# Optimization experiments

Hardware: AMD Instinct MI355X
Metric: run time of the kernel (lower is better)

Reference implementation:

```python
import jax, jax.numpy as jnp
import numpy as np

B, L, D, K, H = 2, 384, 1024, 128, 32
NUM_EDGES = 25600
NUM_T = 1000
SCALING = K ** -0.5
SQRT_2PI = float(np.sqrt(2.0 * np.pi))


def setup_inputs() -> dict:
    key = jax.random.key(0)
    ks = jax.random.split(key, 20)
    s = 0.02
    inp = {}
    inp["token_id"] = jax.random.randint(ks[0], (B, L), 0, 160)
    inp["is_periodic"] = jnp.zeros((B,), dtype=bool)
    inp["pos"] = 5.0 * jax.random.normal(ks[1], (B, L, 3), dtype=jnp.float32)
    inp["adj"] = jnp.ones((B, L, L), dtype=bool)
    inp["node_type_edge"] = jax.random.randint(ks[2], (B, L, L, 2), 0, NUM_EDGES)
    inp["time_step"] = jax.random.uniform(ks[3], (B, L), dtype=jnp.float32)
    inp["clean_mask"] = jnp.zeros((B, L), dtype=bool)
    # parameters
    inp["embed_w"] = s * jax.random.normal(ks[4], (160, D), dtype=jnp.float32)
    inp["Wpos"] = s * jax.random.normal(ks[5], (K, 3), dtype=jnp.float32)
    inp["Wpfe"] = s * jax.random.normal(ks[6], (D, K), dtype=jnp.float32)
    inp["gbf_means"] = jax.random.normal(ks[7], (K,), dtype=jnp.float32)
    inp["gbf_stds"] = 0.5 + jax.random.uniform(ks[8], (K,), dtype=jnp.float32)
    inp["gbf_mul"] = 1.0 + s * jax.random.normal(ks[9], (NUM_EDGES, 1), dtype=jnp.float32)
    inp["gbf_bias"] = s * jax.random.normal(ks[10], (NUM_EDGES, 1), dtype=jnp.float32)
    inp["W1"] = s * jax.random.normal(ks[11], (K, K), dtype=jnp.float32)
    inp["b1"] = jnp.zeros((K,), dtype=jnp.float32)
    inp["W2"] = s * jax.random.normal(ks[12], (H, K), dtype=jnp.float32)
    inp["b2"] = jnp.zeros((H,), dtype=jnp.float32)
    inp["Wproj"] = s * jax.random.normal(ks[13], (D, K), dtype=jnp.float32)
    inp["bproj"] = jnp.zeros((D,), dtype=jnp.float32)
    inp["Wt1"] = s * jax.random.normal(ks[14], (D, D), dtype=jnp.float32)
    inp["bt1"] = jnp.zeros((D,), dtype=jnp.float32)
    inp["Wt2"] = s * jax.random.normal(ks[15], (D, D), dtype=jnp.float32)
    inp["bt2"] = jnp.zeros((D,), dtype=jnp.float32)
    return inp


def _forward(token_id, is_periodic, pos, adj, node_type_edge, time_step, clean_mask,
             embed_w, Wpos, Wpfe, gbf_means, gbf_stds, gbf_mul, gbf_bias,
             W1, b1, W2, b2, Wproj, bproj, Wt1, bt1, Wt2, bt2):
    padding_mask = token_id == 0                                  # (B,L)
    molecule_mask = (token_id <= 129) & (~is_periodic[:, None])   # (B,L)
    x = embed_w[token_id]                                         # (B,L,D)

    # ---- _pos_emb (non-PBC branch: expand_pos = pos, expand_mask = padding_mask) ----
    delta = pos[:, :, None, :] - pos[:, None, :, :]               # (B,L,L,3)
    dist = jnp.sqrt(jnp.maximum(jnp.sum(delta * delta, -1), 1e-12))  # (B,L,L), safe norm

    # GaussianLayer
    mul = gbf_mul[node_type_edge].sum(-2)                         # (B,L,L,1)
    bias = gbf_bias[node_type_edge].sum(-2)                       # (B,L,L,1)
    y = mul * dist[..., None] + bias                              # (B,L,L,1) -> broadcast K
    std = jnp.abs(gbf_stds) + 1e-5
    a = (y - gbf_means) / std
    edge_feature = jnp.exp(-0.5 * a * a) / (SQRT_2PI * std)       # (B,L,L,K)

    # NonLinear projection to per-head bias
    gab = jax.nn.gelu(edge_feature @ W1.T + b1, approximate=False) @ W2.T + b2  # (B,L,L,H)
    gab = jnp.where(padding_mask[:, None, :, None], -jnp.inf, gab)  # expand-col mask
    gab = jnp.where(padding_mask[:, :, None, None], 0.0, gab)       # padding-row mask
    pos_attn_bias = jnp.transpose(gab, (0, 3, 1, 2))              # (B,H,L,L)

    d = gab.sum(-1)                                               # (B,L,L) sum over heads
    minv = jnp.finfo(jnp.float32).min
    d = jnp.where(padding_mask[:, None, :], minv, d)
    d = jnp.where(padding_mask[:, :, None], minv, d)
    adj_eff = adj | (~molecule_mask[:, :, None])
    d = jnp.where(~adj_eff, minv, d)
    attn = jax.nn.softmax(d * SCALING, axis=-1)                   # (B,L,L)

    pos_e = pos @ Wpos.T                                          # (B,L,K)
    pos_e = jnp.where(padding_mask[..., None], 0.0, pos_e)
    pfe = jnp.einsum('bij,bjk->bik', attn, pos_e)                 # (B,L,K)
    pfe = pfe @ Wpfe.T                                            # (B,L,D)

    ef = jnp.where(padding_mask[:, None, :, None], 0.0, edge_feature).sum(-2)  # (B,L,K)
    pfe = pfe + ef @ Wproj.T + bproj
    pos_embedding = jnp.where(padding_mask[..., None], 0.0, pfe)  # (B,L,D)

    # ---- time step encoder (sinusoidal + MLP) ----
    t = jnp.where(clean_mask, 0.0, time_step) * NUM_T             # (B,L)
    half = D // 2
    freqs = jnp.exp(-jnp.log(10000.0) * jnp.arange(half, dtype=jnp.float32) / half)
    ang = t[..., None] * freqs                                    # (B,L,half)
    sin_emb = jnp.concatenate([jnp.sin(ang), jnp.cos(ang)], -1)   # (B,L,D)
    time_embed = jax.nn.silu(sin_emb @ Wt1.T + bt1) @ Wt2.T + bt2

    x = x + time_embed + pos_embedding
    return x, padding_mask, time_embed, pos_attn_bias, pos_embedding


def reference(token_id, is_periodic, pos, adj, node_type_edge, time_step, clean_mask,
              embed_w, Wpos, Wpfe, gbf_means, gbf_stds, gbf_mul, gbf_bias,
              W1, b1, W2, b2, Wproj, bproj, Wt1, bt1, Wt2, bt2):
    return _forward(token_id, is_periodic, pos, adj, node_type_edge, time_step, clean_mask,
                    embed_w, Wpos, Wpfe, gbf_means, gbf_stds, gbf_mul, gbf_bias,
                    W1, b1, W2, b2, Wproj, bproj, Wt1, bt1, Wt2, bt2)
```

## Files before the change

### kernel.cpp

```cpp
#include <hip/hip_runtime.h>
#include <stddef.h>

#define B_ 2
#define L_ 384
#define D_ 1024
#define K_ 128
#define H_ 32

#define MINV (-3.402823466e38f)
#define NEG_BIG (-1.0e38f)
#define SCALING_ 0.08838834764831845f
#define INV_SQRT_2PI 0.3989422804014327f

typedef __attribute__((ext_vector_type(8))) short bf16x8;
typedef __attribute__((ext_vector_type(4))) float f32x4;

__device__ __forceinline__ float finitize(float x) {
    return fminf(fmaxf(x, -1.0e38f), 1.0e38f);
}
__device__ __forceinline__ unsigned short f2bf(float x) {
    unsigned int u = __float_as_uint(x);
    u += 0x7FFFu + ((u >> 16) & 1u);
    return (unsigned short)(u >> 16);
}
__device__ __forceinline__ unsigned short f2bf_rtz(float x) {
    return (unsigned short)(__float_as_uint(x) >> 16);
}
__device__ __forceinline__ float gelu_tanh(float x) {
    const float x2 = x * x;
    const float z = x * fmaf(0.0356774081f, x2, 0.7978845608f);
    const float e = __expf(2.0f * z);
    const float t = fmaf(-2.0f, __builtin_amdgcn_rcpf(e + 1.0f), 1.0f);
    const float hx = 0.5f * x;
    return fmaf(hx, t, hx);
}

__global__ __launch_bounds__(256) void prep_sin_kernel(
    const float* __restrict__ W1, const float* __restrict__ W2,
    const float* __restrict__ Wpfe, const float* __restrict__ Wproj,
    const float* __restrict__ Wt2,
    unsigned short* __restrict__ W1bf, unsigned short* __restrict__ W2bf,
    unsigned short* __restrict__ Wpfebf, unsigned short* __restrict__ Wprojbf,
    unsigned short* __restrict__ Wt2bf,
    const float* __restrict__ time_step, const unsigned char* __restrict__ clean,
    const int* __restrict__ token, unsigned short* __restrict__ sin_bf,
    float* __restrict__ padout)
{
    const int blk = blockIdx.x;
    if (blk < 1300) {
        const int i = blk * 256 + threadIdx.x;
        const float* src; unsigned short* dst; int off;
        if (i < 4096)       { src = W1;    dst = W1bf;    off = i; }
        else if (i < 5120)  { src = W2;    dst = W2bf;    off = i - 4096; }
        else if (i < 37888) { src = Wpfe;  dst = Wpfebf;  off = i - 5120; }
        else if (i < 70656) { src = Wproj; dst = Wprojbf; off = i - 37888; }
        else                { src = Wt2;   dst = Wt2bf;   off = i - 70656; }
        const float4 v = ((const float4*)src)[off];
        ushort4 p; p.x = f2bf(v.x); p.y = f2bf(v.y); p.z = f2bf(v.z); p.w = f2bf(v.w);
        ((ushort4*)dst)[off] = p;
    } else {
        const int row = blk - 1300;
        if (threadIdx.x == 0) padout[row] = (token[row] == 0) ? 1.0f : 0.0f;
        const float t = (clean[row] ? 0.0f : time_step[row]) * 1000.0f;
        for (int k = threadIdx.x; k < 512; k += 256) {
            const float f = __expf(-9.210340371976184f * (float)k * (1.0f / 512.0f));
            const float ang = t * f;
            sin_bf[(size_t)row * D_ + k]       = f2bf(__sinf(ang));
            sin_bf[(size_t)row * D_ + 512 + k] = f2bf(__cosf(ang));
        }
    }
}

__device__ __forceinline__ void gemm_ts_body(
    char* smem, int m0, int n0,
    const unsigned short* __restrict__ A, const float* __restrict__ Bw,
    const float* __restrict__ bias, void* __restrict__ Cv,
    int N, int Kd, int act)
{
    unsigned short (*sA)[72] = (unsigned short(*)[72])smem;
    unsigned short (*sB)[72] = (unsigned short(*)[72])(smem + 4608);
    const int tid  = threadIdx.x;
    const int lane = tid & 63;
    const int wave = tid >> 6;
    const int l15  = lane & 15;
    const int quad = lane >> 4;
    const int mt   = wave & 1;
    const int np   = wave >> 1;

    const int ar = tid >> 3, ac = (tid & 7) * 8;
    const int bc4 = (tid & 15) * 4;

    f32x4 acc[2];
#pragma unroll
    for (int t = 0; t < 2; ++t) acc[t] = (f32x4){0.f, 0.f, 0.f, 0.f};

    uint4 ra = *(const uint4*)&A[(size_t)(m0 + ar) * Kd + ac];
    float4 rbv[4];
#pragma unroll
    for (int c = 0; c < 4; ++c)
        rbv[c] = *(const float4*)&Bw[(size_t)(n0 + ((tid + c * 256) >> 4)) * Kd + bc4];

    for (int k0 = 0; k0 < Kd; k0 += 64) {
        *(uint4*)&sA[ar][ac] = ra;
#pragma unroll
        for (int c = 0; c < 4; ++c) {
            ushort4 p;
            p.x = f2bf(rbv[c].x); p.y = f2bf(rbv[c].y);
            p.z = f2bf(rbv[c].z); p.w = f2bf(rbv[c].w);
            *(ushort4*)&sB[(tid + c * 256) >> 4][bc4] = p;
        }
        __syncthreads();
        if (k0 + 64 < Kd) {
            ra = *(const uint4*)&A[(size_t)(m0 + ar) * Kd + k0 + 64 + ac];
#pragma unroll
            for (int c = 0; c < 4; ++c)
                rbv[c] = *(const float4*)&Bw[(size_t)(n0 + ((tid + c * 256) >> 4)) * Kd + k0 + 64 + bc4];
        }
#pragma unroll
        for (int kk = 0; kk < 64; kk += 32) {
            const bf16x8 av = *(const bf16x8*)&sA[mt * 16 + l15][kk + quad * 8];
#pragma unroll
            for (int t = 0; t < 2; ++t) {
                const bf16x8 bv = *(const bf16x8*)&sB[(np * 2 + t) * 16 + l15][kk + quad * 8];
                acc[t] = __builtin_amdgcn_mfma_f32_16x16x32_bf16(av, bv, acc[t], 0, 0, 0);
            }
        }
        __syncthreads();
    }
#pragma unroll
    for (int t = 0; t < 2; ++t) {
        const int nc = n0 + (np * 2 + t) * 16 + l15;
        const float bv = bias[nc];
#pragma unroll
        for (int r = 0; r < 4; ++r) {
            const int mr = m0 + mt * 16 + quad * 4 + r;
            float v = acc[t][r] + bv;
            if (act) {
                v = v / (1.0f + __expf(-v));
                ((unsigned short*)Cv)[(size_t)mr * N + nc] = f2bf(v);
            } else {
                ((float*)Cv)[(size_t)mr * N + nc] = v;
            }
        }
    }
}

__device__ __forceinline__ void edge_body(
    char* smem, int row,
    const int* __restrict__ token_id,
    const unsigned char* __restrict__ is_periodic,
    const float* __restrict__ pos,
    const unsigned char* __restrict__ adj,
    const int* __restrict__ nte,
    const float* __restrict__ gbf_means,
    const float* __restrict__ gbf_stds,
    const float* __restrict__ gbf_mul,
    const float* __restrict__ gbf_bias,
    const float* __restrict__ b1,
    const float* __restrict__ b2,
    const float* __restrict__ Wpos,
    const unsigned short* __restrict__ W1bf,
    const unsigned short* __restrict__ W2bf,
    unsigned short* __restrict__ pfe_bf,
    unsigned short* __restrict__ ef_bf,
    float* __restrict__ out_pab)
{
    const int b = row / L_;
    const int i = row - b * L_;
    const int tid = threadIdx.x;

    const int tok_i = token_id[row];
    if (tok_i == 0) {
        for (int idx = tid; idx < H_ * L_; idx += 256) {
            const int h = idx / L_;
            const int j = idx - h * L_;
            out_pab[((size_t)(b * H_ + h) * L_ + i) * L_ + j] = 0.0f;
        }
        if (tid < K_) {
            pfe_bf[(size_t)row * K_ + tid] = 0;
            ef_bf[(size_t)row * K_ + tid]  = 0;
        }
        return;
    }

    typedef unsigned short efbuf_t[32][136];
    efbuf_t* sEF = (efbuf_t*)smem;
    unsigned short (*sACT)[136] = (unsigned short(*)[136])(smem + 17408);
    float (*sGab)[33] = (float(*)[33])(smem + 26112);
    float* sD      = (float*)(smem + 30336);
    float* sRed    = (float*)(smem + 31872);
    float* sYall   = (float*)(smem + 32896);
    unsigned char* sPadCol = (unsigned char*)(smem + 34432);

    for (int j = tid; j < L_; j += 256)
        sPadCol[j] = (token_id[b * L_ + j] == 0) ? 1 : 0;

    const float px = pos[(size_t)row * 3 + 0];
    const float py = pos[(size_t)row * 3 + 1];
    const float pz = pos[(size_t)row * 3 + 2];
    for (int jg2 = tid; jg2 < L_; jg2 += 256) {
        const float dx = px - pos[(size_t)(b * L_ + jg2) * 3 + 0];
        const float dy = py - pos[(size_t)(b * L_ + jg2) * 3 + 1];
        const float dz = pz - pos[(size_t)(b * L_ + jg2) * 3 + 2];
        const float dist = sqrtf(fmaxf(dx * dx + dy * dy + dz * dz, 1e-12f));
        const size_t eoff = ((size_t)(b * L_ + i) * L_ + jg2) * 2;
        const int e0 = nte[eoff], e1 = nte[eoff + 1];
        sYall[jg2] = (gbf_mul[e0] + gbf_mul[e1]) * dist + (gbf_bias[e0] + gbf_bias[e1]);
    }

    const int lane = tid & 63;
    const int wave = tid >> 6;
    const int l15  = lane & 15;
    const int quad = lane >> 4;
    const int mt   = wave & 1;
    const int ntb  = (wave >> 1) * 4;
    float rb1[4];
#pragma unroll
    for (int nt = 0; nt < 4; ++nt) rb1[nt] = b1[(ntb + nt) * 16 + l15];
    const int hc = (wave >> 1) * 16 + l15;
    const float rb2 = b2[hc];
    bf16x8 w1f[4][4];
#pragma unroll
    for (int ks = 0; ks < 4; ++ks)
#pragma unroll
        for (int nt = 0; nt < 4; ++nt)
            w1f[ks][nt] = *(const bf16x8*)&W1bf[((ntb + nt) * 16 + l15) * K_ + ks * 32 + quad * 8];
    bf16x8 bv2[4];
#pragma unroll
    for (int ks = 0; ks < 4; ++ks)
        bv2[ks] = *(const bf16x8*)&W2bf[hc * K_ + ks * 32 + quad * 8];

    const int kg4 = (tid & 31) * 4;
    const int jg  = tid >> 5;
    const int jb  = jg * 4;
    float meanv[4], istdv[4], cKv[4];
#pragma unroll
    for (int c = 0; c < 4; ++c) {
        meanv[c] = gbf_means[kg4 + c];
        const float s = fabsf(gbf_stds[kg4 + c]) + 1e-5f;
        istdv[c] = 1.0f / s;
        cKv[c]   = INV_SQRT_2PI * istdv[c];
    }
    float efs[4] = {0.f, 0.f, 0.f, 0.f};

    __syncthreads();

#pragma unroll
    for (int jj = 0; jj < 4; ++jj) {
        const int j = jb + jj;
        const float y = sYall[j];
        const bool ok = !sPadCol[j];
        ushort4 p;
#pragma unroll
        for (int c = 0; c < 4; ++c) {
            const float a = (y - meanv[c]) * istdv[c];
            const float ef = __expf(-0.5f * a * a) * cKv[c];
            ((unsigned short*)&p)[c] = f2bf_rtz(ef);
            if (ok) efs[c] += ef;
        }
        *(ushort4*)&sEF[0][j][kg4] = p;
    }
    __syncthreads();

    for (int tile = 0; tile < L_ / 32; ++tile) {
        const int jt0 = tile * 32;
        const int cur = tile & 1, nxt = cur ^ 1;

        f32x4 acc1[4];
#pragma unroll
        for (int nt = 0; nt < 4; ++nt) acc1[nt] = (f32x4){0.f, 0.f, 0.f, 0.f};
#pragma unroll
        for (int ks = 0; ks < 4; ++ks) {
            const bf16x8 av = *(const bf16x8*)&sEF[cur][mt * 16 + l15][ks * 32 + quad * 8];
#pragma unroll
            for (int nt = 0; nt < 4; ++nt)
                acc1[nt] = __builtin_amdgcn_mfma_f32_16x16x32_bf16(av, w1f[ks][nt], acc1[nt], 0, 0, 0);
        }

        if (tile + 1 < L_ / 32) {
            const int jn0 = jt0 + 32;
#pragma unroll
            for (int jj = 0; jj < 4; ++jj) {
                const int j = jb + jj;
                const float y = sYall[jn0 + j];
                const bool ok = !sPadCol[jn0 + j];
                ushort4 p;
#pragma unroll
                for (int c = 0; c < 4; ++c) {
                    const float a = (y - meanv[c]) * istdv[c];
                    const float ef = __expf(-0.5f * a * a) * cKv[c];
                    ((unsigned short*)&p)[c] = f2bf_rtz(ef);
                    if (ok) efs[c] += ef;
                }
                *(ushort4*)&sEF[nxt][j][kg4] = p;
            }
        }

#pragma unroll
        for (int nt = 0; nt < 4; ++nt) {
            const int kkc = (ntb + nt) * 16 + l15;
#pragma unroll
            for (int r = 0; r < 4; ++r) {
                const float v = gelu_tanh(acc1[nt][r] + rb1[nt]);
                sACT[mt * 16 + quad * 4 + r][kkc] = f2bf_rtz(v);
            }
        }
        __syncthreads();

        f32x4 acc2 = (f32x4){0.f, 0.f, 0.f, 0.f};
#pragma unroll
        for (int ks = 0; ks < 4; ++ks) {
            const bf16x8 av = *(const bf16x8*)&sACT[mt * 16 + l15][ks * 32 + quad * 8];
            acc2 = __builtin_amdgcn_mfma_f32_16x16x32_bf16(av, bv2[ks], acc2, 0, 0, 0);
        }
        const int jl0 = mt * 16 + quad * 4;
#pragma unroll
        for (int r = 0; r < 4; ++r) sGab[jl0 + r][hc] = acc2[r] + rb2;
        __syncthreads();

        {
            const int h = tid >> 3, f = tid & 7;
            const int jb2 = f * 4;
            float4 st;
#pragma unroll
            for (int r = 0; r < 4; ++r) {
                float v = finitize(sGab[jb2 + r][h]);
                if (sPadCol[jt0 + jb2 + r]) v = NEG_BIG;
                ((float*)&st)[r] = v;
            }
            *(float4*)&out_pab[((size_t)(b * H_ + h) * L_ + i) * L_ + jt0 + jb2] = st;
        }
        if (tid < 32) {
            float s = 0.0f;
#pragma unroll
            for (int h = 0; h < 32; ++h) s += sGab[tid][h];
            sD[jt0 + tid] = s;
        }
    }

    {
        float* efScr = (float*)sACT;
#pragma unroll
        for (int c = 0; c < 4; ++c) efScr[jg * 128 + kg4 + c] = efs[c];
    }
    __syncthreads();
    if (tid < 128) {
        const float* efScr = (const float*)sACT;
        float s = 0.0f;
#pragma unroll
        for (int g = 0; g < 8; ++g) s += efScr[g * 128 + tid];
        ef_bf[(size_t)row * K_ + tid] = f2bf(s);
    }
    __syncthreads();

    const bool molecule = (tok_i <= 129) && (is_periodic[b] == 0);
    float lmax = -INFINITY;
    for (int j = tid; j < L_; j += 256) {
        const bool colpad = sPadCol[j] != 0;
        const bool adj_eff = (adj[((size_t)(b * L_ + i)) * L_ + j] != 0) || (!molecule);
        const float dv = (colpad || !adj_eff) ? MINV : sD[j];
        const float s = dv * SCALING_;
        sD[j] = s;
        lmax = fmaxf(lmax, s);
    }
#pragma unroll
    for (int off = 32; off > 0; off >>= 1) lmax = fmaxf(lmax, __shfl_xor(lmax, off));
    if (lane == 0) sRed[wave] = lmax;
    __syncthreads();
    const float smax = fmaxf(fmaxf(sRed[0], sRed[1]), fmaxf(sRed[2], sRed[3]));
    float lsum = 0.0f;
    for (int j = tid; j < L_; j += 256) {
        const float e = __expf(sD[j] - smax);
        sD[j] = e;
        lsum += e;
    }
#pragma unroll
    for (int off = 32; off > 0; off >>= 1) lsum += __shfl_xor(lsum, off);
    if (lane == 0) sRed[4 + wave] = lsum;
    __syncthreads();
    const float inv = 1.0f / (sRed[4] + sRed[5] + sRed[6] + sRed[7]);

    float a0 = 0.f, a1 = 0.f, a2 = 0.f;
    for (int j = tid; j < L_; j += 256) {
        if (!sPadCol[j]) {
            const float e = sD[j];
            a0 += e * pos[(size_t)(b * L_ + j) * 3 + 0];
            a1 += e * pos[(size_t)(b * L_ + j) * 3 + 1];
            a2 += e * pos[(size_t)(b * L_ + j) * 3 + 2];
        }
    }
#pragma unroll
    for (int off = 32; off > 0; off >>= 1) {
        a0 += __shfl_xor(a0, off);
        a1 += __shfl_xor(a1, off);
        a2 += __shfl_xor(a2, off);
    }
    if (lane == 0) { sRed[8 + wave] = a0; sRed[12 + wave] = a1; sRed[16 + wave] = a2; }
    __syncthreads();
    if (tid < 128) {
        const float m0 = sRed[8] + sRed[9] + sRed[10] + sRed[11];
        const float m1 = sRed[12] + sRed[13] + sRed[14] + sRed[15];
        const float m2 = sRed[16] + sRed[17] + sRed[18] + sRed[19];
        const float w0 = Wpos[tid * 3 + 0], w1 = Wpos[tid * 3 + 1], w2 = Wpos[tid * 3 + 2];
        pfe_bf[(size_t)row * K_ + tid] = f2bf((m0 * w0 + m1 * w1 + m2 * w2) * inv);
    }
}

__global__ __launch_bounds__(256, 3) void edge_ts1(
    const int* __restrict__ token_id,
    const unsigned char* __restrict__ is_periodic,
    const float* __restrict__ pos,
    const unsigned char* __restrict__ adj,
    const int* __restrict__ nte,
    const float* __restrict__ gbf_means,
    const float* __restrict__ gbf_stds,
    const float* __restrict__ gbf_mul,
    const float* __restrict__ gbf_bias,
    const float* __restrict__ b1,
    const float* __restrict__ b2,
    const float* __restrict__ Wpos,
    const unsigned short* __restrict__ W1bf,
    const unsigned short* __restrict__ W2bf,
    unsigned short* __restrict__ pfe_bf,
    unsigned short* __restrict__ ef_bf,
    float* __restrict__ out_pab,
    const unsigned short* __restrict__ sin_bf,
    const float* __restrict__ Wt1,
    const float* __restrict__ bt1,
    unsigned short* __restrict__ h1_bf)
{
    __shared__ __align__(16) char smem[34816];
    const int bx = blockIdx.x;
    if (bx < B_ * L_) {
        edge_body(smem, bx, token_id, is_periodic, pos, adj, nte,
                  gbf_means, gbf_stds, gbf_mul, gbf_bias, b1, b2, Wpos,
                  W1bf, W2bf, pfe_bf, ef_bf, out_pab);
    } else {
        const int tsb = bx - B_ * L_;
        const int m0 = (tsb >> 4) * 32;
        const int n0 = (tsb & 15) * 64;
        gemm_ts_body(smem, m0, n0, sin_bf, Wt1, bt1, (void*)h1_bf, D_, D_, 1);
    }
}

__global__ __launch_bounds__(256) void ts2_pe_kernel(
    const unsigned short* __restrict__ h1_bf,
    const unsigned short* __restrict__ Wt2bf,
    const float* __restrict__ bt2,
    const unsigned short* __restrict__ pfe_bf,
    const unsigned short* __restrict__ ef_bf,
    const unsigned short* __restrict__ Wpfebf,
    const unsigned short* __restrict__ Wprojbf,
    const float* __restrict__ bproj,
    const int* __restrict__ token,
    const float* __restrict__ embed_w,
    float* __restrict__ outTE,
    float* __restrict__ outPE,
    float* __restrict__ outX)
{
    __shared__ __align__(16) char smem[17408];
    const int tid  = threadIdx.x;
    const int lane = tid & 63;
    const int wave = tid >> 6;
    const int l15  = lane & 15;
    const int quad = lane >> 4;
    const int mt   = wave & 1;
    const int np   = wave >> 1;
    const int m0 = blockIdx.y * 32, n0 = blockIdx.x * 32;

    f32x4 accTE = (f32x4){0.f, 0.f, 0.f, 0.f};
    {
        unsigned short (*sA)[72] = (unsigned short(*)[72])smem;
        unsigned short (*sB)[72] = (unsigned short(*)[72])(smem + 4608);
        const int ar = tid >> 3, ac = (tid & 7) * 8;

        uint4 ra = *(const uint4*)&h1_bf[(size_t)(m0 + ar) * D_ + ac];
        uint4 rb = *(const uint4*)&Wt2bf[(size_t)(n0 + ar) * D_ + ac];

        for (int k0 = 0; k0 < D_; k0 += 64) {
            *(uint4*)&sA[ar][ac] = ra;
            *(uint4*)&sB[ar][ac] = rb;
            __syncthreads();
            if (k0 + 64 < D_) {
                ra = *(const uint4*)&h1_bf[(size_t)(m0 + ar) * D_ + k0 + 64 + ac];
                rb = *(const uint4*)&Wt2bf[(size_t)(n0 + ar) * D_ + k0 + 64 + ac];
            }
#pragma unroll
            for (int kk = 0; kk < 64; kk += 32) {
                const bf16x8 av = *(const bf16x8*)&sA[mt * 16 + l15][kk + quad * 8];
                const bf16x8 bv = *(const bf16x8*)&sB[np * 16 + l15][kk + quad * 8];
                accTE = __builtin_amdgcn_mfma_f32_16x16x32_bf16(av, bv, accTE, 0, 0, 0);
            }
            __syncthreads();
        }
    }

    unsigned short (*sA2)[136] = (unsigned short(*)[136])smem;
    unsigned short (*sB2)[136] = (unsigned short(*)[136])(smem + 8704);
    f32x4 accPE = (f32x4){0.f, 0.f, 0.f, 0.f};

    for (int phase = 0; phase < 2; ++phase) {
        const unsigned short* Ap = phase ? ef_bf : pfe_bf;
        const unsigned short* Bp = phase ? Wprojbf : Wpfebf;
#pragma unroll
        for (int e = tid; e < 512; e += 256) {
            const int r = e >> 4, c8 = (e & 15) * 8;
            *(uint4*)&sA2[r][c8] = *(const uint4*)&Ap[(size_t)(m0 + r) * K_ + c8];
        }
#pragma unroll
        for (int e = tid; e < 512; e += 256) {
            const int r = e >> 4, c8 = (e & 15) * 8;
            *(uint4*)&sB2[r][c8] = *(const uint4*)&Bp[(size_t)(n0 + r) * K_ + c8];
        }
        __syncthreads();
#pragma unroll
        for (int ks = 0; ks < 4; ++ks) {
            const bf16x8 av = *(const bf16x8*)&sA2[mt * 16 + l15][ks * 32 + quad * 8];
            const bf16x8 bv = *(const bf16x8*)&sB2[np * 16 + l15][ks * 32 + quad * 8];
            accPE = __builtin_amdgcn_mfma_f32_16x16x32_bf16(av, bv, accPE, 0, 0, 0);
        }
        __syncthreads();
    }

    {
        const int nc = n0 + np * 16 + l15;
        const float bte = bt2[nc];
        const float bpe = bproj[nc];
#pragma unroll
        for (int r = 0; r < 4; ++r) {
            const int mr = m0 + mt * 16 + quad * 4 + r;
            const int tok = token[mr];
            const float te = accTE[r] + bte;
            const float pe = (tok == 0) ? 0.0f : (accPE[r] + bpe);
            outTE[(size_t)mr * D_ + nc] = te;
            outPE[(size_t)mr * D_ + nc] = pe;
            outX[(size_t)mr * D_ + nc] = embed_w[(size_t)tok * D_ + nc] + te + pe;
        }
    }
}

extern "C" void kernel_launch(void* const* d_in, const int* in_sizes, int n_in,
                              void* d_out, int out_size, void* d_ws, size_t ws_size,
                              hipStream_t stream) {
    const int*           token_id    = (const int*)d_in[0];
    const unsigned char* is_periodic = (const unsigned char*)d_in[1];
    const float*         pos         = (const float*)d_in[2];
    const unsigned char* adj         = (const unsigned char*)d_in[3];
    const int*           nte         = (const int*)d_in[4];
    const float*         time_step   = (const float*)d_in[5];
    const unsigned char* clean_mask  = (const unsigned char*)d_in[6];
    const float*         embed_w     = (const float*)d_in[7];
    const float*         Wpos        = (const float*)d_in[8];
    const float*         Wpfe        = (const float*)d_in[9];
    const float*         gbf_means   = (const float*)d_in[10];
    const float*         gbf_stds    = (const float*)d_in[11];
    const float*         gbf_mul     = (const float*)d_in[12];
    const float*         gbf_bias    = (const float*)d_in[13];
    const float*         W1          = (const float*)d_in[14];
    const float*         b1          = (const float*)d_in[15];
    const float*         W2          = (const float*)d_in[16];
    const float*         b2          = (const float*)d_in[17];
    const float*         Wproj       = (const float*)d_in[18];
    const float*         bproj       = (const float*)d_in[19];
    const float*         Wt1         = (const float*)d_in[20];
    const float*         bt1         = (const float*)d_in[21];
    const float*         Wt2         = (const float*)d_in[22];
    const float*         bt2         = (const float*)d_in[23];

    float* out = (float*)d_out;
    float* out_x   = out;
    float* out_pad = out + 786432;
    float* out_te  = out + 787200;
    float* out_pab = out + 1573632;
    float* out_pe  = out + 11010816;

    unsigned short* wsu = (unsigned short*)d_ws;
    unsigned short* W1bf    = wsu;
    unsigned short* W2bf    = wsu + 16384;
    unsigned short* Wpfebf  = wsu + 20480;
    unsigned short* Wprojbf = wsu + 151552;
    unsigned short* Wt2bf   = wsu + 282624;
    unsigned short* sin_bf  = wsu + 1331200;
    unsigned short* h1_bf   = wsu + 2117632;
    unsigned short* pfe_bf  = wsu + 2904064;
    unsigned short* ef_bf   = wsu + 3002368;

    prep_sin_kernel<<<dim3(2068), dim3(256), 0, stream>>>(
        W1, W2, Wpfe, Wproj, Wt2, W1bf, W2bf, Wpfebf, Wprojbf, Wt2bf,
        time_step, clean_mask, token_id, sin_bf, out_pad);
    edge_ts1<<<dim3(B_ * L_ + 384), dim3(256), 0, stream>>>(
        token_id, is_periodic, pos, adj, nte, gbf_means, gbf_stds, gbf_mul, gbf_bias,
        b1, b2, Wpos, W1bf, W2bf, pfe_bf, ef_bf, out_pab,
        sin_bf, Wt1, bt1, h1_bf);
    ts2_pe_kernel<<<dim3(32, 24), dim3(256), 0, stream>>>(
        h1_bf, Wt2bf, bt2, pfe_bf, ef_bf, Wpfebf, Wprojbf, bproj, token_id, embed_w,
        out_te, out_pe, out_x);
}
```

Before: 182.8 us.

## Fold prep kernel into edge/ts1 launch, generate sinusoids inside GEMM

Removes the separate prep kernel. The sinusoidal time embedding is now computed on the fly inside the first time-step GEMM's A-tile load instead of being materialized to a bf16 workspace. W1/W2 are converted to bf16 directly in registers in the edge blocks, and the remaining weight conversions run as extra blocks of the same launch. This saves one launch and a global round trip for the sin buffer, at the cost of redundant exp/sin/cos work per N-tile and extra conversion work in each edge block.

```diff
diff --git a/kernel.cpp b/kernel.cpp
--- a/kernel.cpp
+++ b/kernel.cpp
@@ -34,48 +34,23 @@
     const float hx = 0.5f * x;
     return fmaf(hx, t, hx);
 }
-
-__global__ __launch_bounds__(256) void prep_sin_kernel(
-    const float* __restrict__ W1, const float* __restrict__ W2,
-    const float* __restrict__ Wpfe, const float* __restrict__ Wproj,
-    const float* __restrict__ Wt2,
-    unsigned short* __restrict__ W1bf, unsigned short* __restrict__ W2bf,
-    unsigned short* __restrict__ Wpfebf, unsigned short* __restrict__ Wprojbf,
-    unsigned short* __restrict__ Wt2bf,
-    const float* __restrict__ time_step, const unsigned char* __restrict__ clean,
-    const int* __restrict__ token, unsigned short* __restrict__ sin_bf,
-    float* __restrict__ padout)
-{
-    const int blk = blockIdx.x;
-    if (blk < 1300) {
-        const int i = blk * 256 + threadIdx.x;
-        const float* src; unsigned short* dst; int off;
-        if (i < 4096)       { src = W1;    dst = W1bf;    off = i; }
-        else if (i < 5120)  { src = W2;    dst = W2bf;    off = i - 4096; }
-        else if (i < 37888) { src = Wpfe;  dst = Wpfebf;  off = i - 5120; }
-        else if (i < 70656) { src = Wproj; dst = Wprojbf; off = i - 37888; }
-        else                { src = Wt2;   dst = Wt2bf;   off = i - 70656; }
-        const float4 v = ((const float4*)src)[off];
-        ushort4 p; p.x = f2bf(v.x); p.y = f2bf(v.y); p.z = f2bf(v.z); p.w = f2bf(v.w);
-        ((ushort4*)dst)[off] = p;
-    } else {
-        const int row = blk - 1300;
-        if (threadIdx.x == 0) padout[row] = (token[row] == 0) ? 1.0f : 0.0f;
-        const float t = (clean[row] ? 0.0f : time_step[row]) * 1000.0f;
-        for (int k = threadIdx.x; k < 512; k += 256) {
-            const float f = __expf(-9.210340371976184f * (float)k * (1.0f / 512.0f));
-            const float ang = t * f;
-            sin_bf[(size_t)row * D_ + k]       = f2bf(__sinf(ang));
-            sin_bf[(size_t)row * D_ + 512 + k] = f2bf(__cosf(ang));
-        }
-    }
+__device__ __forceinline__ bf16x8 cvt8(const float* __restrict__ src) {
+    const float4 a = *(const float4*)src;
+    const float4 b = *(const float4*)(src + 4);
+    bf16x8 r;
+    r[0] = (short)f2bf(a.x); r[1] = (short)f2bf(a.y);
+    r[2] = (short)f2bf(a.z); r[3] = (short)f2bf(a.w);
+    r[4] = (short)f2bf(b.x); r[5] = (short)f2bf(b.y);
+    r[6] = (short)f2bf(b.z); r[7] = (short)f2bf(b.w);
+    return r;
 }
 
 __device__ __forceinline__ void gemm_ts_body(
     char* smem, int m0, int n0,
-    const unsigned short* __restrict__ A, const float* __restrict__ Bw,
-    const float* __restrict__ bias, void* __restrict__ Cv,
-    int N, int Kd, int act)
+    const float* __restrict__ time_step, const unsigned char* __restrict__ clean,
+    const float* __restrict__ Bw,
+    const float* __restrict__ bias, unsigned short* __restrict__ Cbf,
+    int N, int Kd)
 {
     unsigned short (*sA)[72] = (unsigned short(*)[72])smem;
     unsigned short (*sB)[72] = (unsigned short(*)[72])(smem + 4608);
@@ -90,18 +65,35 @@
     const int ar = tid >> 3, ac = (tid & 7) * 8;
     const int bc4 = (tid & 15) * 4;
 
+    const int arow = m0 + ar;
+    const float t = (clean[arow] ? 0.0f : time_step[arow]) * 1000.0f;
+
     f32x4 acc[2];
 #pragma unroll
-    for (int t = 0; t < 2; ++t) acc[t] = (f32x4){0.f, 0.f, 0.f, 0.f};
-
-    uint4 ra = *(const uint4*)&A[(size_t)(m0 + ar) * Kd + ac];
+    for (int t2 = 0; t2 < 2; ++t2) acc[t2] = (f32x4){0.f, 0.f, 0.f, 0.f};
+
     float4 rbv[4];
 #pragma unroll
     for (int c = 0; c < 4; ++c)
         rbv[c] = *(const float4*)&Bw[(size_t)(n0 + ((tid + c * 256) >> 4)) * Kd + bc4];
 
     for (int k0 = 0; k0 < Kd; k0 += 64) {
-        *(uint4*)&sA[ar][ac] = ra;
+        {
+            const int kbase = k0 + ac;
+            ushort4 p0, p1;
+#pragma unroll
+            for (int e = 0; e < 8; ++e) {
+                const int k = kbase + e;
+                const int km = (k < 512) ? k : (k - 512);
+                const float f = __expf(-9.210340371976184f * (float)km * (1.0f / 512.0f));
+                const float ang = t * f;
+                const float v = (k < 512) ? __sinf(ang) : __cosf(ang);
+                if (e < 4) ((unsigned short*)&p0)[e] = f2bf(v);
+                else       ((unsigned short*)&p1)[e - 4] = f2bf(v);
+            }
+            *(ushort4*)&sA[ar][ac]     = p0;
+            *(ushort4*)&sA[ar][ac + 4] = p1;
+        }
 #pragma unroll
         for (int c = 0; c < 4; ++c) {
             ushort4 p;
@@ -111,7 +103,6 @@
         }
         __syncthreads();
         if (k0 + 64 < Kd) {
-            ra = *(const uint4*)&A[(size_t)(m0 + ar) * Kd + k0 + 64 + ac];
 #pragma unroll
             for (int c = 0; c < 4; ++c)
                 rbv[c] = *(const float4*)&Bw[(size_t)(n0 + ((tid + c * 256) >> 4)) * Kd + k0 + 64 + bc4];
@@ -120,27 +111,23 @@
         for (int kk = 0; kk < 64; kk += 32) {
             const bf16x8 av = *(const bf16x8*)&sA[mt * 16 + l15][kk + quad * 8];
 #pragma unroll
-            for (int t = 0; t < 2; ++t) {
-                const bf16x8 bv = *(const bf16x8*)&sB[(np * 2 + t) * 16 + l15][kk + quad * 8];
-                acc[t] = __builtin_amdgcn_mfma_f32_16x16x32_bf16(av, bv, acc[t], 0, 0, 0);
+            for (int t2 = 0; t2 < 2; ++t2) {
+                const bf16x8 bv = *(const bf16x8*)&sB[(np * 2 + t2) * 16 + l15][kk + quad * 8];
+                acc[t2] = __builtin_amdgcn_mfma_f32_16x16x32_bf16(av, bv, acc[t2], 0, 0, 0);
             }
         }
         __syncthreads();
     }
 #pragma unroll
-    for (int t = 0; t < 2; ++t) {
-        const int nc = n0 + (np * 2 + t) * 16 + l15;
+    for (int t2 = 0; t2 < 2; ++t2) {
+        const int nc = n0 + (np * 2 + t2) * 16 + l15;
         const float bv = bias[nc];
 #pragma unroll
         for (int r = 0; r < 4; ++r) {
             const int mr = m0 + mt * 16 + quad * 4 + r;
-            float v = acc[t][r] + bv;
-            if (act) {
-                v = v / (1.0f + __expf(-v));
-                ((unsigned short*)Cv)[(size_t)mr * N + nc] = f2bf(v);
-            } else {
-                ((float*)Cv)[(size_t)mr * N + nc] = v;
-            }
+            float v = acc[t2][r] + bv;
+            v = v / (1.0f + __expf(-v));
+            Cbf[(size_t)mr * N + nc] = f2bf(v);
         }
     }
 }
@@ -159,17 +146,19 @@
     const float* __restrict__ b1,
     const float* __restrict__ b2,
     const float* __restrict__ Wpos,
-    const unsigned short* __restrict__ W1bf,
-    const unsigned short* __restrict__ W2bf,
+    const float* __restrict__ W1,
+    const float* __restrict__ W2,
     unsigned short* __restrict__ pfe_bf,
     unsigned short* __restrict__ ef_bf,
-    float* __restrict__ out_pab)
+    float* __restrict__ out_pab,
+    float* __restrict__ out_pad)
 {
     const int b = row / L_;
     const int i = row - b * L_;
     const int tid = threadIdx.x;
 
     const int tok_i = token_id[row];
+    if (tid == 0) out_pad[row] = (tok_i == 0) ? 1.0f : 0.0f;
     if (tok_i == 0) {
         for (int idx = tid; idx < H_ * L_; idx += 256) {
             const int h = idx / L_;
@@ -224,11 +213,11 @@
     for (int ks = 0; ks < 4; ++ks)
 #pragma unroll
         for (int nt = 0; nt < 4; ++nt)
-            w1f[ks][nt] = *(const bf16x8*)&W1bf[((ntb + nt) * 16 + l15) * K_ + ks * 32 + quad * 8];
+            w1f[ks][nt] = cvt8(&W1[(size_t)((ntb + nt) * 16 + l15) * K_ + ks * 32 + quad * 8]);
     bf16x8 bv2[4];
 #pragma unroll
     for (int ks = 0; ks < 4; ++ks)
-        bv2[ks] = *(const bf16x8*)&W2bf[hc * K_ + ks * 32 + quad * 8];
+        bv2[ks] = cvt8(&W2[(size_t)hc * K_ + ks * 32 + quad * 8]);
 
     const int kg4 = (tid & 31) * 4;
     const int jg  = tid >> 5;
@@ -419,27 +408,44 @@
     const float* __restrict__ b1,
     const float* __restrict__ b2,
     const float* __restrict__ Wpos,
-    const unsigned short* __restrict__ W1bf,
-    const unsigned short* __restrict__ W2bf,
+    const float* __restrict__ W1,
+    const float* __restrict__ W2,
     unsigned short* __restrict__ pfe_bf,
     unsigned short* __restrict__ ef_bf,
     float* __restrict__ out_pab,
-    const unsigned short* __restrict__ sin_bf,
+    float* __restrict__ out_pad,
+    const float* __restrict__ time_step,
+    const unsigned char* __restrict__ clean_mask,
     const float* __restrict__ Wt1,
     const float* __restrict__ bt1,
-    unsigned short* __restrict__ h1_bf)
+    unsigned short* __restrict__ h1_bf,
+    const float* __restrict__ Wpfe,
+    const float* __restrict__ Wproj,
+    const float* __restrict__ Wt2,
+    unsigned short* __restrict__ Wpfebf,
+    unsigned short* __restrict__ Wprojbf,
+    unsigned short* __restrict__ Wt2bf)
 {
     __shared__ __align__(16) char smem[34816];
     const int bx = blockIdx.x;
     if (bx < B_ * L_) {
         edge_body(smem, bx, token_id, is_periodic, pos, adj, nte,
                   gbf_means, gbf_stds, gbf_mul, gbf_bias, b1, b2, Wpos,
-                  W1bf, W2bf, pfe_bf, ef_bf, out_pab);
-    } else {
+                  W1, W2, pfe_bf, ef_bf, out_pab, out_pad);
+    } else if (bx < B_ * L_ + 384) {
         const int tsb = bx - B_ * L_;
         const int m0 = (tsb >> 4) * 32;
         const int n0 = (tsb & 15) * 64;
-        gemm_ts_body(smem, m0, n0, sin_bf, Wt1, bt1, (void*)h1_bf, D_, D_, 1);
+        gemm_ts_body(smem, m0, n0, time_step, clean_mask, Wt1, bt1, h1_bf, D_, D_);
+    } else {
+        const int i = (bx - (B_ * L_ + 384)) * 256 + threadIdx.x;
+        const float* src; unsigned short* dst; int off;
+        if (i < 32768)      { src = Wpfe;  dst = Wpfebf;  off = i; }
+        else if (i < 65536) { src = Wproj; dst = Wprojbf; off = i - 32768; }
+        else                { src = Wt2;   dst = Wt2bf;   off = i - 65536; }
+        const float4 v = ((const float4*)src)[off];
+        ushort4 p; p.x = f2bf(v.x); p.y = f2bf(v.y); p.z = f2bf(v.z); p.w = f2bf(v.w);
+        ((ushort4*)dst)[off] = p;
     }
 }
 
@@ -575,23 +581,18 @@
     float* out_pe  = out + 11010816;
 
     unsigned short* wsu = (unsigned short*)d_ws;
-    unsigned short* W1bf    = wsu;
-    unsigned short* W2bf    = wsu + 16384;
     unsigned short* Wpfebf  = wsu + 20480;
     unsigned short* Wprojbf = wsu + 151552;
     unsigned short* Wt2bf   = wsu + 282624;
-    unsigned short* sin_bf  = wsu + 1331200;
     unsigned short* h1_bf   = wsu + 2117632;
     unsigned short* pfe_bf  = wsu + 2904064;
     unsigned short* ef_bf   = wsu + 3002368;
 
-    prep_sin_kernel<<<dim3(2068), dim3(256), 0, stream>>>(
-        W1, W2, Wpfe, Wproj, Wt2, W1bf, W2bf, Wpfebf, Wprojbf, Wt2bf,
-        time_step, clean_mask, token_id, sin_bf, out_pad);
-    edge_ts1<<<dim3(B_ * L_ + 384), dim3(256), 0, stream>>>(
+    edge_ts1<<<dim3(B_ * L_ + 384 + 1280), dim3(256), 0, stream>>>(
         token_id, is_periodic, pos, adj, nte, gbf_means, gbf_stds, gbf_mul, gbf_bias,
-        b1, b2, Wpos, W1bf, W2bf, pfe_bf, ef_bf, out_pab,
-        sin_bf, Wt1, bt1, h1_bf);
+        b1, b2, Wpos, W1, W2, pfe_bf, ef_bf, out_pab, out_pad,
+        time_step, clean_mask, Wt1, bt1, h1_bf,
+        Wpfe, Wproj, Wt2, Wpfebf, Wprojbf, Wt2bf);
     ts2_pe_kernel<<<dim3(32, 24), dim3(256), 0, stream>>>(
         h1_bf, Wt2bf, bt2, pfe_bf, ef_bf, Wpfebf, Wprojbf, bproj, token_id, embed_w,
         out_te, out_pe, out_x);
```

New measurement: 201.1 us. 10.0% more time.
